# Kernel optimization log

Hardware: AMD Instinct MI355X
Metric: run time of the kernel (lower is better)

Reference implementation:

```python
import jax, jax.numpy as jnp
import numpy as np

NUM_EMBEDDINGS = 1024
EMBEDDING_DIM = 64
COMMITMENT_COST = 0.1
DECAY = 0.9
EPSILON = 1e-05


def setup_inputs() -> dict:
    key = jax.random.key(0)
    k1, k2, k3 = jax.random.split(key, 3)
    inputs = jax.random.normal(k1, (16, EMBEDDING_DIM, 4096), dtype=jnp.float32)
    embedding_weight = jax.random.normal(k2, (NUM_EMBEDDINGS, EMBEDDING_DIM), dtype=jnp.float32)
    ema_cluster_size = jnp.zeros((NUM_EMBEDDINGS,), dtype=jnp.float32)
    ema_w = jax.random.normal(k3, (NUM_EMBEDDINGS, EMBEDDING_DIM), dtype=jnp.float32)
    return {
        "inputs": inputs,
        "embedding_weight": embedding_weight,
        "ema_cluster_size": ema_cluster_size,
        "ema_w": ema_w,
    }


def reference(inputs, embedding_weight, ema_cluster_size, ema_w):
    K, D = embedding_weight.shape
    # (B, C, L) -> (B, L, C); C == embedding_dim
    x = jnp.transpose(inputs, (0, 2, 1))
    B, L, _ = x.shape
    flat = x.reshape(-1, D)  # [N, D], N = B*L
    N = flat.shape[0]

    distances = (
        jnp.sum(flat * flat, axis=1, keepdims=True)
        + jnp.sum(embedding_weight * embedding_weight, axis=1)
        - 2.0 * (flat @ embedding_weight.T)
    )
    idx = jnp.argmin(distances, axis=1)  # [N] int

    # embedding lookup (equivalent to one-hot @ weight)
    quantized = embedding_weight[idx].reshape(B, L, D)

    # one-hot column sums and scatter-reduction, without materializing [N, K]
    counts = jnp.zeros((K,), dtype=flat.dtype).at[idx].add(1.0)  # sum(encodings, 0)
    dw = jax.ops.segment_sum(flat, idx, num_segments=K)  # encodings^T @ flat_input

    # EMA updates (training path)
    cs = ema_cluster_size * DECAY + (1.0 - DECAY) * counts
    n = jnp.sum(cs)
    cs = (cs + EPSILON) / (n + K * EPSILON) * n
    new_ema_w = ema_w * DECAY + (1.0 - DECAY) * dw
    new_embedding_weight = new_ema_w / cs[:, None]

    # KLDivLoss(batchmean)(softmax(quantized.detach()), softmax(inputs)) over dim=2
    p_in = jax.nn.softmax(jax.lax.stop_gradient(quantized), axis=2)
    p_tgt = jax.nn.softmax(x, axis=2)
    kl = jnp.sum(p_tgt * (jnp.log(p_tgt) - p_in)) / B
    loss = COMMITMENT_COST * kl

    # straight-through estimator
    quantized_st = x + jax.lax.stop_gradient(quantized - x)

    avg_probs = counts / N
    perplexity = jnp.exp(-jnp.sum(avg_probs * jnp.log(avg_probs + 1e-10)))

    out = jnp.transpose(quantized_st, (0, 2, 1))  # back to (B, C, L)
    encoding_indices = idx[:, None]
    return (out, loss, perplexity, new_embedding_weight, encoding_indices)
```

## Files before the change

kernel.cpp:

```cpp
#include <hip/hip_runtime.h>

#define LDIM 4096
#define DDIM 64
#define KCODES 1024
#define BDIM 16
#define NROWS 65536
#define NSLICE 8
#define SLICE_ROWS (NROWS / NSLICE)

typedef __attribute__((ext_vector_type(8))) short short8;
typedef __attribute__((ext_vector_type(16))) float float16v;

__device__ __forceinline__ unsigned int orderf(float f) {
  unsigned int u = __float_as_uint(f);
  return (u & 0x80000000u) ? ~u : (u | 0x80000000u);
}

__device__ __forceinline__ unsigned long long shfl_xor_u64(unsigned long long v, int m) {
  int lo = __shfl_xor((int)(unsigned int)(v & 0xffffffffull), m, 64);
  int hi = __shfl_xor((int)(unsigned int)(v >> 32), m, 64);
  return ((unsigned long long)(unsigned int)hi << 32) | (unsigned int)lo;
}

__device__ __forceinline__ unsigned int bf16_rne(float x) {
  unsigned int u = __float_as_uint(x);
  return (u + 0x7FFFu + ((u >> 16) & 1u)) >> 16;
}

__global__ void prep_kernel(const float* __restrict__ Ew,
                            float* __restrict__ enorm,
                            float* __restrict__ SE,
                            unsigned short* __restrict__ Epk2) {
  int k = blockIdx.x;
  int d = threadIdx.x;
  float v = Ew[k * DDIM + d];
  float n2 = v * v;
  #pragma unroll
  for (int o = 32; o > 0; o >>= 1) n2 += __shfl_xor(n2, o, 64);
  float m = v;
  #pragma unroll
  for (int o = 32; o > 0; o >>= 1) m = fmaxf(m, __shfl_xor(m, o, 64));
  float e = expf(v - m);
  float Z = e;
  #pragma unroll
  for (int o = 32; o > 0; o >>= 1) Z += __shfl_xor(Z, o, 64);
  SE[k * DDIM + d] = e / Z;
  if (d == 0) enorm[k] = n2;

  unsigned int rh = bf16_rne(v);
  float hif = __uint_as_float(rh << 16);
  unsigned int rl = bf16_rne(v - hif);
  int tile = k >> 5, mm = k & 31;
  int s = d >> 4, h = (d >> 3) & 1, j = d & 7;
  int base = tile * 4096 + (h * 32 + mm) * 8 + j;
  Epk2[base + s * 512]        = (unsigned short)rh;
  Epk2[base + (4 + s) * 512]  = (unsigned short)rl;
}

__launch_bounds__(256, 2)
__global__ void argmin_fused_kernel(const float* __restrict__ inp,
                                    const unsigned short* __restrict__ Epk2,
                                    const float* __restrict__ enorm,
                                    const float* __restrict__ Ew,
                                    const float* __restrict__ SE,
                                    int* __restrict__ idx_ws,
                                    float* __restrict__ outidx,
                                    float* __restrict__ out,
                                    float* __restrict__ klacc) {
  __shared__ int kbuf[4][32];

  const int tid = threadIdx.x;
  const int lane = tid & 63;
  const int w = tid >> 6;
  const int half = lane >> 5;
  const int m = lane & 31;
  const int row_base = blockIdx.x * 128 + w * 32;
  const int b = row_base >> 12;
  const int l0 = row_base & 4095;
  const float* xp = inp + (size_t)b * DDIM * LDIM + l0 + m;
  float* op = out + (size_t)b * DDIM * LDIM + l0 + m;

  float xr[32];
  short8 afr[8];
  #pragma unroll
  for (int s = 0; s < 4; s++) {
    #pragma unroll
    for (int j = 0; j < 8; j++) {
      int d = 16 * s + 8 * half + j;
      float x = xp[(size_t)d * LDIM];
      xr[s * 8 + j] = x;
      unsigned int rh = bf16_rne(x);
      float hif = __uint_as_float(rh << 16);
      unsigned int rl = bf16_rne(x - hif);
      afr[s][j] = (short)(unsigned short)rh;
      afr[4 + s][j] = (short)(unsigned short)rl;
    }
  }

  float bsc[16];
  int bix[16];
  #pragma unroll
  for (int j = 0; j < 16; j++) { bsc[j] = 1e30f; bix[j] = 0; }

  const unsigned short* eb = Epk2 + lane * 8;

  short8 bA[8], bB[8];
  float enA, enB;

  #pragma unroll
  for (int s = 0; s < 4; s++) {
    bA[s]     = *(const short8*)(eb + s * 512);
    bA[4 + s] = *(const short8*)(eb + 2048 + s * 512);
  }
  enA = enorm[m];

  #pragma unroll 1
  for (int i = 0; i < 16; i++) {
    const int tB = 2 * i + 1;
    {
      const unsigned short* p = eb + tB * 4096;
      #pragma unroll
      for (int s = 0; s < 4; s++) {
        bB[s]     = *(const short8*)(p + s * 512);
        bB[4 + s] = *(const short8*)(p + 2048 + s * 512);
      }
      enB = enorm[tB * 32 + m];
    }
    {
      float16v a0 = {}, a1 = {}, a2 = {};
      #pragma unroll
      for (int s = 0; s < 4; s++) {
        a0 = __builtin_amdgcn_mfma_f32_32x32x16_bf16(afr[s], bA[s], a0, 0, 0, 0);
        a1 = __builtin_amdgcn_mfma_f32_32x32x16_bf16(afr[s], bA[4 + s], a1, 0, 0, 0);
        a2 = __builtin_amdgcn_mfma_f32_32x32x16_bf16(afr[4 + s], bA[s], a2, 0, 0, 0);
      }
      int ci = 2 * i * 32 + m;
      #pragma unroll
      for (int j = 0; j < 16; j++) {
        float sc = fmaf(-2.f, a0[j] + a1[j] + a2[j], enA);
        if (sc < bsc[j]) { bsc[j] = sc; bix[j] = ci; }
      }
    }
    if (i < 15) {
      const unsigned short* p = eb + (2 * i + 2) * 4096;
      #pragma unroll
      for (int s = 0; s < 4; s++) {
        bA[s]     = *(const short8*)(p + s * 512);
        bA[4 + s] = *(const short8*)(p + 2048 + s * 512);
      }
      enA = enorm[(2 * i + 2) * 32 + m];
    }
    {
      float16v a0 = {}, a1 = {}, a2 = {};
      #pragma unroll
      for (int s = 0; s < 4; s++) {
        a0 = __builtin_amdgcn_mfma_f32_32x32x16_bf16(afr[s], bB[s], a0, 0, 0, 0);
        a1 = __builtin_amdgcn_mfma_f32_32x32x16_bf16(afr[s], bB[4 + s], a1, 0, 0, 0);
        a2 = __builtin_amdgcn_mfma_f32_32x32x16_bf16(afr[4 + s], bB[s], a2, 0, 0, 0);
      }
      int ci = tB * 32 + m;
      #pragma unroll
      for (int j = 0; j < 16; j++) {
        float sc = fmaf(-2.f, a0[j] + a1[j] + a2[j], enB);
        if (sc < bsc[j]) { bsc[j] = sc; bix[j] = ci; }
      }
    }
  }

  #pragma unroll
  for (int j = 0; j < 16; j++) {
    unsigned long long key =
        ((unsigned long long)orderf(bsc[j]) << 32) | (unsigned int)bix[j];
    #pragma unroll
    for (int mm = 1; mm < 32; mm <<= 1) {
      unsigned long long o = shfl_xor_u64(key, mm);
      if (o < key) key = o;
    }
    if (m == 0) {
      int row_local = (j & 3) + 8 * (j >> 2) + 4 * half;
      int grow = row_base + row_local;
      int cidx = (int)(key & 0xffffffffull);
      idx_ws[grow] = cidx;
      outidx[grow] = (float)cidx;
      kbuf[w][row_local] = cidx;
    }
  }

  const int km = kbuf[w][m];

  const float* SEk = SE + km * DDIM + 8 * half;
  const float* Ewk = Ew + km * DDIM + 8 * half;
  float Zh = 0.f, S1h = 0.f, Uh = 0.f;
  #pragma unroll
  for (int s = 0; s < 4; s++) {
    float qv[8], ev[8];
    *(float4*)&qv[0] = *(const float4*)(SEk + 16 * s);
    *(float4*)&qv[4] = *(const float4*)(SEk + 16 * s + 4);
    *(float4*)&ev[0] = *(const float4*)(Ewk + 16 * s);
    *(float4*)&ev[4] = *(const float4*)(Ewk + 16 * s + 4);
    #pragma unroll
    for (int j = 0; j < 8; j++) {
      float x = xr[s * 8 + j];
      float e = expf(x);
      Zh += e;
      S1h += e * x;
      Uh += e * qv[j];
      op[(size_t)(16 * s + 8 * half + j) * LDIM] = ev[j];
    }
  }
  float Zt = Zh + __shfl_xor(Zh, 32, 64);
  float S1t = S1h + __shfl_xor(S1h, 32, 64);
  float Ut = Uh + __shfl_xor(Uh, 32, 64);
  float kl = (half == 0) ? ((S1t - Ut) / Zt - logf(Zt)) : 0.f;
  #pragma unroll
  for (int o = 32; o > 0; o >>= 1) kl += __shfl_xor(kl, o, 64);
  if (lane == 0) atomicAdd(klacc, kl);
}

__launch_bounds__(512)
__global__ void dw_partial_kernel(const float* __restrict__ inp,
                                  const int* __restrict__ idx_ws,
                                  float* __restrict__ partial,
                                  float* __restrict__ pcounts) {
  __shared__ float dwp[KCODES];
  __shared__ float cnt[KCODES];
  const int d = blockIdx.x & 63;
  const int slice = blockIdx.x >> 6;
  const int tid = threadIdx.x;
  const bool do_cnt = (d == 0);

  #pragma unroll
  for (int i = 0; i < KCODES / 512; i++) {
    dwp[tid + i * 512] = 0.f;
    cnt[tid + i * 512] = 0.f;
  }
  __syncthreads();

  const int r0 = slice * SLICE_ROWS;
  for (int i = tid; i < SLICE_ROWS; i += 512) {
    int r = r0 + i;
    int b = r >> 12, l = r & 4095;
    float x = inp[(size_t)b * DDIM * LDIM + (size_t)d * LDIM + l];
    int k = idx_ws[r];
    atomicAdd(&dwp[k], x);
    if (do_cnt) atomicAdd(&cnt[k], 1.0f);
  }
  __syncthreads();

  float* dst = partial + ((size_t)slice * 64 + d) * KCODES;
  #pragma unroll
  for (int i = 0; i < KCODES / 512; i++) dst[tid + i * 512] = dwp[tid + i * 512];
  if (do_cnt) {
    float* cd = pcounts + (size_t)slice * KCODES;
    #pragma unroll
    for (int i = 0; i < KCODES / 512; i++) cd[tid + i * 512] = cnt[tid + i * 512];
  }
}

__global__ void csp_kernel(const float* __restrict__ ema_cs,
                           const float* __restrict__ pcounts,
                           float* __restrict__ csp,
                           float* __restrict__ perp_out) {
  __shared__ float red1[16], red2[16];
  int k = threadIdx.x;
  float c = 0.f;
  #pragma unroll
  for (int sl = 0; sl < NSLICE; sl++) c += pcounts[sl * KCODES + k];
  float cs = ema_cs[k] * 0.9f + 0.1f * c;
  float n = cs;
  #pragma unroll
  for (int o = 32; o > 0; o >>= 1) n += __shfl_xor(n, o, 64);
  if ((k & 63) == 0) red1[k >> 6] = n;
  float a = c * (1.0f / 65536.0f);
  float ent = a * logf(a + 1e-10f);
  float es = ent;
  #pragma unroll
  for (int o = 32; o > 0; o >>= 1) es += __shfl_xor(es, o, 64);
  if ((k & 63) == 0) red2[k >> 6] = es;
  __syncthreads();
  if (k == 0) {
    float t1 = 0.f, t2 = 0.f;
    for (int i = 0; i < 16; i++) { t1 += red1[i]; t2 += red2[i]; }
    red1[0] = t1;
    *perp_out = expf(-t2);
  }
  __syncthreads();
  float N = red1[0];
  csp[k] = (cs + 1e-5f) / (N + 1024.0f * 1e-5f) * N;
}

__launch_bounds__(256)
__global__ void reduce_embed_kernel(const float* __restrict__ partial,
                                    const float* __restrict__ emaw,
                                    const float* __restrict__ csp,
                                    const float* __restrict__ klacc,
                                    float* __restrict__ emb_out,
                                    float* __restrict__ loss_out) {
  int i = blockIdx.x * 256 + threadIdx.x;
  int k = i >> 6, d = i & 63;
  float s = 0.f;
  #pragma unroll
  for (int sl = 0; sl < NSLICE; sl++)
    s += partial[((size_t)sl * 64 + d) * KCODES + k];
  float v = fmaf(0.1f, s, emaw[i] * 0.9f);
  emb_out[i] = v / csp[k];
  if (i == 0) *loss_out = 0.1f * (*klacc) * (1.0f / 16.0f);
}

extern "C" void kernel_launch(void* const* d_in, const int* in_sizes, int n_in,
                              void* d_out, int out_size, void* d_ws, size_t ws_size,
                              hipStream_t stream) {
  const float* inp   = (const float*)d_in[0];
  const float* Ew    = (const float*)d_in[1];
  const float* emacs = (const float*)d_in[2];
  const float* emaw  = (const float*)d_in[3];

  float* out      = (float*)d_out;
  float* loss_out = out + 4194304;
  float* perp_out = out + 4194305;
  float* emb_out  = out + 4194306;
  float* idxf_out = out + 4194306 + 65536;

  char* ws = (char*)d_ws;
  int*   idx_ws  = (int*)(ws);
  float* klacc   = (float*)(ws + 262144);
  float* enorm   = (float*)(ws + 266496);
  float* csp     = (float*)(ws + 270592);
  float* SE      = (float*)(ws + 274688);
  unsigned short* Epk2 = (unsigned short*)(ws + 536832);
  float* partial = (float*)(ws + 536832);
  float* pcounts = (float*)(ws + 2633984);

  hipMemsetAsync(ws + 262144, 0, 256, stream);

  prep_kernel<<<KCODES, 64, 0, stream>>>(Ew, enorm, SE, Epk2);
  argmin_fused_kernel<<<512, 256, 0, stream>>>(inp, Epk2, enorm, Ew, SE,
                                               idx_ws, idxf_out, out, klacc);
  dw_partial_kernel<<<64 * NSLICE, 512, 0, stream>>>(inp, idx_ws, partial, pcounts);
  csp_kernel<<<1, 1024, 0, stream>>>(emacs, pcounts, csp, perp_out);
  reduce_embed_kernel<<<NROWS / 256, 256, 0, stream>>>(partial, emaw, csp, klacc,
                                                       emb_out, loss_out);
}
```

Baseline: 189.6 us.

## Stage codebook tiles through double-buffered LDS via direct global-to-LDS loads

Instead of each wave loading the packed bf16 codebook fragments straight from global memory into registers, the block cooperatively copies 4 tiles at a time into a double-buffered LDS staging area using global_load_lds. The next chunk is fetched while the current one is consumed, and the codebook norms are also cached in LDS. This shares codebook traffic across the four waves of a block and cuts redundant global/L2 reads. In exchange it adds about 66KB of LDS per block, which may limit occupancy below the launch bound of 2, and adds a barrier per chunk.

```diff
diff --git a/kernel.cpp b/kernel.cpp
--- a/kernel.cpp
+++ b/kernel.cpp
@@ -25,6 +25,12 @@
 __device__ __forceinline__ unsigned int bf16_rne(float x) {
   unsigned int u = __float_as_uint(x);
   return (u + 0x7FFFu + ((u >> 16) & 1u)) >> 16;
+}
+
+__device__ __forceinline__ void gl_lds16(const void* g, void* l) {
+  __builtin_amdgcn_global_load_lds(
+      (const __attribute__((address_space(1))) void*)g,
+      (__attribute__((address_space(3))) void*)l, 16, 0, 0);
 }
 
 __global__ void prep_kernel(const float* __restrict__ Ew,
@@ -67,6 +73,8 @@
                                     float* __restrict__ outidx,
                                     float* __restrict__ out,
                                     float* __restrict__ klacc) {
+  __shared__ unsigned short slots[2][16384];
+  __shared__ float ens[KCODES];
   __shared__ int kbuf[4][32];
 
   const int tid = threadIdx.x;
@@ -80,6 +88,18 @@
   const float* xp = inp + (size_t)b * DDIM * LDIM + l0 + m;
   float* op = out + (size_t)b * DDIM * LDIM + l0 + m;
 
+  {
+    const char* src = (const char*)Epk2 + w * 8192 + (lane << 4);
+    char* dst = (char*)&slots[0][0] + w * 8192;
+    #pragma unroll
+    for (int q = 0; q < 8; q++)
+      gl_lds16(src + q * 1024, dst + q * 1024);
+  }
+  {
+    float4 v = ((const float4*)enorm)[tid];
+    *(float4*)&ens[tid << 2] = v;
+  }
+
   float xr[32];
   short8 afr[8];
   #pragma unroll
@@ -96,72 +116,50 @@
       afr[4 + s][j] = (short)(unsigned short)rl;
     }
   }
+  __syncthreads();
 
   float bsc[16];
   int bix[16];
   #pragma unroll
   for (int j = 0; j < 16; j++) { bsc[j] = 1e30f; bix[j] = 0; }
 
-  const unsigned short* eb = Epk2 + lane * 8;
-
-  short8 bA[8], bB[8];
-  float enA, enB;
-
-  #pragma unroll
-  for (int s = 0; s < 4; s++) {
-    bA[s]     = *(const short8*)(eb + s * 512);
-    bA[4 + s] = *(const short8*)(eb + 2048 + s * 512);
-  }
-  enA = enorm[m];
-
   #pragma unroll 1
-  for (int i = 0; i < 16; i++) {
-    const int tB = 2 * i + 1;
-    {
-      const unsigned short* p = eb + tB * 4096;
+  for (int i = 0; i < 8; i++) {
+    asm volatile("s_waitcnt vmcnt(0)" ::: "memory");
+    __builtin_amdgcn_s_barrier();
+    if (i < 7) {
+      const char* src = (const char*)Epk2 + (i + 1) * 32768 + w * 8192 + (lane << 4);
+      char* dst = (char*)&slots[(i + 1) & 1][0] + w * 8192;
+      #pragma unroll
+      for (int q = 0; q < 8; q++)
+        gl_lds16(src + q * 1024, dst + q * 1024);
+    }
+    const unsigned short* cur = &slots[i & 1][0];
+
+    #pragma unroll
+    for (int tile = 0; tile < 4; tile++) {
+      const int gt = i * 4 + tile;
+      const int ci = gt * 32 + m;
+      const float en = ens[ci];
+      const unsigned short* tb = cur + tile * 4096 + lane * 8;
+
+      short8 bfr[8];
       #pragma unroll
       for (int s = 0; s < 4; s++) {
-        bB[s]     = *(const short8*)(p + s * 512);
-        bB[4 + s] = *(const short8*)(p + 2048 + s * 512);
+        bfr[s]     = *(const short8*)(tb + s * 512);
+        bfr[4 + s] = *(const short8*)(tb + 2048 + s * 512);
       }
-      enB = enorm[tB * 32 + m];
-    }
-    {
+
       float16v a0 = {}, a1 = {}, a2 = {};
       #pragma unroll
       for (int s = 0; s < 4; s++) {
-        a0 = __builtin_amdgcn_mfma_f32_32x32x16_bf16(afr[s], bA[s], a0, 0, 0, 0);
-        a1 = __builtin_amdgcn_mfma_f32_32x32x16_bf16(afr[s], bA[4 + s], a1, 0, 0, 0);
-        a2 = __builtin_amdgcn_mfma_f32_32x32x16_bf16(afr[4 + s], bA[s], a2, 0, 0, 0);
+        a0 = __builtin_amdgcn_mfma_f32_32x32x16_bf16(afr[s], bfr[s], a0, 0, 0, 0);
+        a1 = __builtin_amdgcn_mfma_f32_32x32x16_bf16(afr[s], bfr[4 + s], a1, 0, 0, 0);
+        a2 = __builtin_amdgcn_mfma_f32_32x32x16_bf16(afr[4 + s], bfr[s], a2, 0, 0, 0);
       }
-      int ci = 2 * i * 32 + m;
       #pragma unroll
       for (int j = 0; j < 16; j++) {
-        float sc = fmaf(-2.f, a0[j] + a1[j] + a2[j], enA);
-        if (sc < bsc[j]) { bsc[j] = sc; bix[j] = ci; }
-      }
-    }
-    if (i < 15) {
-      const unsigned short* p = eb + (2 * i + 2) * 4096;
-      #pragma unroll
-      for (int s = 0; s < 4; s++) {
-        bA[s]     = *(const short8*)(p + s * 512);
-        bA[4 + s] = *(const short8*)(p + 2048 + s * 512);
-      }
-      enA = enorm[(2 * i + 2) * 32 + m];
-    }
-    {
-      float16v a0 = {}, a1 = {}, a2 = {};
-      #pragma unroll
-      for (int s = 0; s < 4; s++) {
-        a0 = __builtin_amdgcn_mfma_f32_32x32x16_bf16(afr[s], bB[s], a0, 0, 0, 0);
-        a1 = __builtin_amdgcn_mfma_f32_32x32x16_bf16(afr[s], bB[4 + s], a1, 0, 0, 0);
-        a2 = __builtin_amdgcn_mfma_f32_32x32x16_bf16(afr[4 + s], bB[s], a2, 0, 0, 0);
-      }
-      int ci = tB * 32 + m;
-      #pragma unroll
-      for (int j = 0; j < 16; j++) {
-        float sc = fmaf(-2.f, a0[j] + a1[j] + a2[j], enB);
+        float sc = fmaf(-2.f, a0[j] + a1[j] + a2[j], en);
         if (sc < bsc[j]) { bsc[j] = sc; bix[j] = ci; }
       }
     }
```

New measurement: 197.8 us. 1.04x slower.
